# Performance work log

Hardware: AMD Instinct MI355X
Metric: run time of the kernel (lower is better)

The kernel has to match this reference:

```python
import jax, jax.numpy as jnp
import numpy as np

NUM_HEADS = 32
NUM_KV_HEADS = 32
HEAD_DIM = 128
SCALE = 0.08838834764831845  # 1/sqrt(128)
B = 4096
NUM_SLOTS = 32768


def setup_inputs() -> dict:
    key = jax.random.key(0)
    kq, kk, kv, kkc, kvc, ks = jax.random.split(key, 6)
    D_q = NUM_HEADS * HEAD_DIM
    D_kv = NUM_KV_HEADS * HEAD_DIM
    q = jax.random.normal(kq, (B, D_q), dtype=jnp.float32)
    k = jax.random.normal(kk, (B, D_kv), dtype=jnp.float32)
    v = jax.random.normal(kv, (B, D_kv), dtype=jnp.float32)
    k_cache = jax.random.normal(kkc, (NUM_SLOTS, D_kv), dtype=jnp.float32)
    v_cache = jax.random.normal(kvc, (NUM_SLOTS, D_kv), dtype=jnp.float32)
    # collision-free slots (real KV caches assign unique slots per token)
    slot_mapping = jax.random.permutation(ks, NUM_SLOTS)[:B].astype(jnp.int64)
    return {"q": q, "k": k, "v": v, "k_cache": k_cache, "v_cache": v_cache,
            "slot_mapping": slot_mapping}


def reference(q, k, v, k_cache, v_cache, slot_mapping):
    b = q.shape[0]
    # store_kvcache: scatter fresh k/v rows into the paged cache
    kc = k_cache.at[slot_mapping].set(k)
    vc = v_cache.at[slot_mapping].set(v)
    # decode path: gather this step's k/v back out of the cache
    kk = kc[slot_mapping].reshape(b, NUM_KV_HEADS, HEAD_DIM)
    vv = vc[slot_mapping].reshape(b, NUM_KV_HEADS, HEAD_DIM)
    qq = q.reshape(b, NUM_HEADS, HEAD_DIM)
    # pytorch_attention: scores over the head axis -> (B, H, Hkv)
    scores = jnp.einsum('bhd,bkd->bhk', qq, kk) * SCALE
    probs = jax.nn.softmax(scores, axis=-1)
    out = jnp.einsum('bhk,bkd->bhd', probs, vv)  # (B, H, D)
    return out.reshape(b, NUM_HEADS * HEAD_DIM)
```

## Files before the change

### kernel.cpp

```cpp
#include <hip/hip_runtime.h>

typedef __bf16 bf16x8 __attribute__((ext_vector_type(8)));
typedef float f32x16 __attribute__((ext_vector_type(16)));
typedef float f32x4  __attribute__((ext_vector_type(4)));
typedef unsigned int u32x4 __attribute__((ext_vector_type(4)));

#define HEAD_DIM 128
#define D_MODEL  4096

__device__ __forceinline__ unsigned pack_bf16(float lo, float hi) {
    unsigned a = (unsigned)__builtin_bit_cast(unsigned short, (__bf16)lo);
    unsigned b = (unsigned)__builtin_bit_cast(unsigned short, (__bf16)hi);
    return a | (b << 16);
}

__global__ __launch_bounds__(256, 4) void attn_kernel(
    const float* __restrict__ q,
    const float* __restrict__ k,
    const float* __restrict__ v,
    float* __restrict__ out)
{
    constexpr float SCALE_LOG2E = 0.08838834764831845f * 1.4426950408889634f;

    const int lane = threadIdx.x & 63;
    const int b    = blockIdx.x * 4 + (threadIdx.x >> 6);
    const int r    = lane & 31;
    const int hi   = lane >> 5;

    const float* qb = q + (size_t)b * D_MODEL;
    const float* kb = k + (size_t)b * D_MODEL;
    const float* vb = v + (size_t)b * D_MODEL;

    f32x16 acc = {};
    const int rowoff = r * HEAD_DIM + hi * 8;
#pragma unroll
    for (int s = 0; s < 8; ++s) {
        const float* qp = qb + rowoff + s * 16;
        const float* kp = kb + rowoff + s * 16;
        f32x4 q0 = *(const f32x4*)(qp);
        f32x4 q1 = *(const f32x4*)(qp + 4);
        f32x4 k0 = *(const f32x4*)(kp);
        f32x4 k1 = *(const f32x4*)(kp + 4);
        bf16x8 aK, bQ;
#pragma unroll
        for (int j = 0; j < 4; ++j) { aK[j] = (__bf16)k0[j]; aK[4 + j] = (__bf16)k1[j]; }
#pragma unroll
        for (int j = 0; j < 4; ++j) { bQ[j] = (__bf16)q0[j]; bQ[4 + j] = (__bf16)q1[j]; }
        acc = __builtin_amdgcn_mfma_f32_32x32x16_bf16(aK, bQ, acc, 0, 0, 0);
    }

    float vf[64];
#pragma unroll
    for (int t = 0; t < 2; ++t)
#pragma unroll
        for (int c = 0; c < 4; ++c) {
            const float* vp = vb + (size_t)(t * 16 + hi * 8) * HEAD_DIM + c * 32 + r;
#pragma unroll
            for (int j = 0; j < 8; ++j)
                vf[t * 32 + c * 8 + j] = vp[(size_t)j * HEAD_DIM];
        }

    float m = acc[0];
#pragma unroll
    for (int i = 1; i < 16; ++i) m = fmaxf(m, acc[i]);
    m = fmaxf(m, __shfl_xor(m, 32, 64));

    float sum = 0.f;
#pragma unroll
    for (int i = 0; i < 16; ++i) {
        acc[i] = __builtin_amdgcn_exp2f((acc[i] - m) * SCALE_LOG2E);
        sum += acc[i];
    }
    sum += __shfl_xor(sum, 32, 64);
    const float inv = __builtin_amdgcn_rcpf(sum);

    unsigned w[8];
#pragma unroll
    for (int i = 0; i < 8; ++i) w[i] = pack_bf16(acc[2 * i] * inv, acc[2 * i + 1] * inv);

    bf16x8 pa[2];
#pragma unroll
    for (int t = 0; t < 2; ++t) {
        unsigned W0 = w[4 * t], W1 = w[4 * t + 1], W2 = w[4 * t + 2], W3 = w[4 * t + 3];
        unsigned X0 = (unsigned)__shfl_xor((int)W0, 32, 64);
        unsigned X1 = (unsigned)__shfl_xor((int)W1, 32, 64);
        unsigned X2 = (unsigned)__shfl_xor((int)W2, 32, 64);
        unsigned X3 = (unsigned)__shfl_xor((int)W3, 32, 64);
        u32x4 wv;
        wv[0] = hi ? X2 : W0;
        wv[1] = hi ? X3 : W1;
        wv[2] = hi ? W2 : X0;
        wv[3] = hi ? W3 : X1;
        pa[t] = __builtin_bit_cast(bf16x8, wv);
    }

    float* ob = out + (size_t)b * D_MODEL;
#pragma unroll
    for (int c = 0; c < 4; ++c) {
        f32x16 oacc = {};
#pragma unroll
        for (int t = 0; t < 2; ++t) {
            bf16x8 bV;
#pragma unroll
            for (int j = 0; j < 8; ++j) bV[j] = (__bf16)vf[t * 32 + c * 8 + j];
            oacc = __builtin_amdgcn_mfma_f32_32x32x16_bf16(pa[t], bV, oacc, 0, 0, 0);
        }
        float* op = ob + c * 32 + r;
#pragma unroll
        for (int reg = 0; reg < 16; ++reg) {
            const int h = (reg & 3) + 8 * (reg >> 2) + 4 * hi;
            op[(size_t)h * HEAD_DIM] = oacc[reg];
        }
    }
}

extern "C" void kernel_launch(void* const* d_in, const int* in_sizes, int n_in,
                              void* d_out, int out_size, void* d_ws, size_t ws_size,
                              hipStream_t stream) {
    const float* q = (const float*)d_in[0];
    const float* k = (const float*)d_in[1];
    const float* v = (const float*)d_in[2];
    float* out = (float*)d_out;
    const int B = in_sizes[0] / D_MODEL;
    attn_kernel<<<dim3(B / 4), dim3(256), 0, stream>>>(q, k, v, out);
}
```

Before: 47.54 us.

## Stage Q and K through swizzled LDS as bf16 with coalesced global loads

Q and K rows are loaded with fully coalesced lane-contiguous float4 reads, converted to bf16 and written to a per-wave LDS region with an XOR swizzle. MFMA operands are then read back from LDS, replacing the strided per-row global reads. Launch bounds drop from 4 to 2 blocks per CU because of the 64KB LDS footprint and the extra registers for the staging arrays. The aim is better global memory coalescing, at the cost of occupancy and LDS round-trips.

After: 44.65 us. 1.06x faster.

```diff
diff --git a/kernel.cpp b/kernel.cpp
--- a/kernel.cpp
+++ b/kernel.cpp
@@ -3,6 +3,7 @@
 typedef __bf16 bf16x8 __attribute__((ext_vector_type(8)));
 typedef float f32x16 __attribute__((ext_vector_type(16)));
 typedef float f32x4  __attribute__((ext_vector_type(4)));
+typedef unsigned int u32x2 __attribute__((ext_vector_type(2)));
 typedef unsigned int u32x4 __attribute__((ext_vector_type(4)));
 
 #define HEAD_DIM 128
@@ -14,7 +15,7 @@
     return a | (b << 16);
 }
 
-__global__ __launch_bounds__(256, 4) void attn_kernel(
+__global__ __launch_bounds__(256, 2) void attn_kernel(
     const float* __restrict__ q,
     const float* __restrict__ k,
     const float* __restrict__ v,
@@ -22,32 +23,24 @@
 {
     constexpr float SCALE_LOG2E = 0.08838834764831845f * 1.4426950408889634f;
 
+    __shared__ u32x4 lds_buf[4096];
+    const int wid  = threadIdx.x >> 6;
     const int lane = threadIdx.x & 63;
-    const int b    = blockIdx.x * 4 + (threadIdx.x >> 6);
-    const int r    = lane & 31;
-    const int hi   = lane >> 5;
+    char* ldsQ = (char*)lds_buf + wid * 16384;
+    char* ldsK = ldsQ + 8192;
+
+    const int b  = blockIdx.x * 4 + wid;
+    const int r  = lane & 31;
+    const int hi = lane >> 5;
 
     const float* qb = q + (size_t)b * D_MODEL;
     const float* kb = k + (size_t)b * D_MODEL;
     const float* vb = v + (size_t)b * D_MODEL;
 
-    f32x16 acc = {};
-    const int rowoff = r * HEAD_DIM + hi * 8;
+    f32x4 qraw[16];
 #pragma unroll
-    for (int s = 0; s < 8; ++s) {
-        const float* qp = qb + rowoff + s * 16;
-        const float* kp = kb + rowoff + s * 16;
-        f32x4 q0 = *(const f32x4*)(qp);
-        f32x4 q1 = *(const f32x4*)(qp + 4);
-        f32x4 k0 = *(const f32x4*)(kp);
-        f32x4 k1 = *(const f32x4*)(kp + 4);
-        bf16x8 aK, bQ;
-#pragma unroll
-        for (int j = 0; j < 4; ++j) { aK[j] = (__bf16)k0[j]; aK[4 + j] = (__bf16)k1[j]; }
-#pragma unroll
-        for (int j = 0; j < 4; ++j) { bQ[j] = (__bf16)q0[j]; bQ[4 + j] = (__bf16)q1[j]; }
-        acc = __builtin_amdgcn_mfma_f32_32x32x16_bf16(aK, bQ, acc, 0, 0, 0);
-    }
+    for (int i = 0; i < 16; ++i)
+        qraw[i] = *(const f32x4*)(qb + i * 256 + lane * 4);
 
     float vf[64];
 #pragma unroll
@@ -59,6 +52,43 @@
             for (int j = 0; j < 8; ++j)
                 vf[t * 32 + c * 8 + j] = vp[(size_t)j * HEAD_DIM];
         }
+
+#pragma unroll
+    for (int i = 0; i < 16; ++i) {
+        const int byteoff = i * 512 + lane * 8;
+        const int row = byteoff >> 8;
+        const int swz = byteoff ^ ((row & 7) << 4);
+        u32x2 w2;
+        w2[0] = pack_bf16(qraw[i][0], qraw[i][1]);
+        w2[1] = pack_bf16(qraw[i][2], qraw[i][3]);
+        *(u32x2*)(ldsQ + swz) = w2;
+    }
+
+    f32x4 kraw[16];
+#pragma unroll
+    for (int i = 0; i < 16; ++i)
+        kraw[i] = *(const f32x4*)(kb + i * 256 + lane * 4);
+
+#pragma unroll
+    for (int i = 0; i < 16; ++i) {
+        const int byteoff = i * 512 + lane * 8;
+        const int row = byteoff >> 8;
+        const int swz = byteoff ^ ((row & 7) << 4);
+        u32x2 w2;
+        w2[0] = pack_bf16(kraw[i][0], kraw[i][1]);
+        w2[1] = pack_bf16(kraw[i][2], kraw[i][3]);
+        *(u32x2*)(ldsK + swz) = w2;
+    }
+
+    f32x16 acc = {};
+#pragma unroll
+    for (int s = 0; s < 8; ++s) {
+        const int fb   = r * 256 + s * 32 + hi * 16;
+        const int fswz = fb ^ ((r & 7) << 4);
+        bf16x8 aK = *(const bf16x8*)(ldsK + fswz);
+        bf16x8 bQ = *(const bf16x8*)(ldsQ + fswz);
+        acc = __builtin_amdgcn_mfma_f32_32x32x16_bf16(aK, bQ, acc, 0, 0, 0);
+    }
 
     float m = acc[0];
 #pragma unroll
```
